# Kernel optimization log

Measured on AMD Instinct MI355X. Metric: run time of the kernel, lower is better.

## Reference

```python
import jax, jax.numpy as jnp
import numpy as np

N = 20000      # total nodes (20 proteins x 1000 residues)
E = 320000     # edges (avg degree 16)
F_IN = 22      # amino-acid feature dim
H = 4          # attention heads
C = 64         # hidden dim per head
HC = H * C     # 256
G = 20         # number of graphs
OUT = 128      # output embedding dim
NEG_SLOPE = 0.2


def setup_inputs() -> dict:
    key = jax.random.key(0)
    ks = jax.random.split(key, 24)
    x = jax.random.normal(ks[0], (N, F_IN), dtype=jnp.float32)
    edge_index = jax.random.randint(ks[1], (2, E), 0, N)
    batch = jnp.arange(N, dtype=jnp.int64) // (N // G)  # 1000 nodes per graph
    s = 0.1
    d = {
        'x': x, 'edge_index': edge_index, 'batch': batch,
        'Win': jax.random.normal(ks[2], (F_IN, C)) * s,
        'bin_': jnp.zeros((C,), jnp.float32),
        'Wout': jax.random.normal(ks[3], (2 * HC, OUT)) * s,
        'bout': jnp.zeros((OUT,), jnp.float32),
    }
    kidx = 4
    for i in range(3):
        in_dim = C if i == 0 else HC
        d[f'Wl{i}'] = jax.random.normal(ks[kidx], (in_dim, HC)) * s; kidx += 1
        d[f'Wr{i}'] = jax.random.normal(ks[kidx], (in_dim, HC)) * s; kidx += 1
        d[f'att{i}'] = jax.random.normal(ks[kidx], (H, C)) * s; kidx += 1
        d[f'b{i}'] = jnp.zeros((HC,), jnp.float32)
    return d


def _gatv2_layer(h, src, dst, Wl, Wr, att, bias):
    # PyG GATv2Conv (share_weights=False, concat=True), dropout off (eval)
    xl = (h @ Wl).reshape(-1, H, C)   # source transform (x_j)
    xr = (h @ Wr).reshape(-1, H, C)   # target transform (x_i)
    e = jax.nn.leaky_relu(xl[src] + xr[dst], NEG_SLOPE)  # [E+N, H, C]
    logit = jnp.einsum('ehc,hc->eh', e, att)             # [E+N, H]
    mx = jax.ops.segment_max(logit, dst, num_segments=N)
    mx = jnp.where(jnp.isfinite(mx), mx, 0.0)
    ex = jnp.exp(logit - mx[dst])
    den = jax.ops.segment_sum(ex, dst, num_segments=N)
    alpha = ex / (den[dst] + 1e-16)                      # segment softmax
    out = jax.ops.segment_sum(alpha[:, :, None] * xl[src], dst, num_segments=N)
    return out.reshape(-1, HC) + bias


def reference(x, edge_index, batch, Win, bin_,
              Wl0, Wr0, att0, b0, Wl1, Wr1, att1, b1, Wl2, Wr2, att2, b2,
              Wout, bout):
    # add self-loops once (add_self_loops=True in every GATv2Conv)
    loops = jnp.arange(N, dtype=edge_index.dtype)
    src = jnp.concatenate([edge_index[0], loops])
    dst = jnp.concatenate([edge_index[1], loops])

    h = jax.nn.relu(x @ Win + bin_)  # input_proj + ReLU (dropout = eval identity)
    layers = [(Wl0, Wr0, att0, b0), (Wl1, Wr1, att1, b1), (Wl2, Wr2, att2, b2)]
    for (Wl, Wr, att, b) in layers:
        h_prev = h
        h = jax.nn.elu(_gatv2_layer(h, src, dst, Wl, Wr, att, b))
        if h_prev.shape[-1] == h.shape[-1]:  # residual when dims match (layers 1,2)
            h = h + h_prev

    counts = jax.ops.segment_sum(jnp.ones((N,), h.dtype), batch, num_segments=G)
    x_mean = jax.ops.segment_sum(h, batch, num_segments=G) / counts[:, None]
    x_max = jax.ops.segment_max(h, batch, num_segments=G)
    x_global = jnp.concatenate([x_mean, x_max], axis=-1)  # [G, 512]
    return x_global @ Wout + bout                          # [G, 128]
```

## Files before the change

### kernel.cpp

```cpp
#include <hip/hip_runtime.h>
#include <hip/hip_bf16.h>
#include <math.h>

#define N_NODES 20000
#define N_EDGES 320000
#define F_IN 22
#define H_HEADS 4
#define C_DIM 64
#define HC 256
#define G_GRAPHS 20
#define OUT_DIM 128
#define NODES_PER_G 1000
#define POOL_CHUNKS 8
#define NODES_PER_CHUNK (NODES_PER_G / POOL_CHUNKS)
#define SCAN_NB ((N_NODES + 255) / 256)

typedef unsigned short ushortT;
typedef __attribute__((ext_vector_type(8))) short short8;
typedef __attribute__((ext_vector_type(4))) float v4f;

__device__ inline ushortT f2bf(float f) {
    unsigned int u = __float_as_uint(f);
    unsigned int r = (u + 0x7fffu + ((u >> 16) & 1u)) >> 16;
    return (ushortT)r;
}

__device__ inline float4 unpack_bf4(uint2 u) {
    float4 f;
    f.x = __uint_as_float(u.x << 16);
    f.y = __uint_as_float(u.x & 0xffff0000u);
    f.z = __uint_as_float(u.y << 16);
    f.w = __uint_as_float(u.y & 0xffff0000u);
    return f;
}


__global__ void hist_kernel(const int* __restrict__ dst, int* __restrict__ cnt, int e) {
    int i = blockIdx.x * blockDim.x + threadIdx.x;
    if (i < e) atomicAdd(&cnt[dst[i]], 1);
}

__global__ __launch_bounds__(256) void scanA_kernel(const int* __restrict__ cnt,
                                                    int* __restrict__ bsum) {
    __shared__ int red[256];
    int b = blockIdx.x, t = threadIdx.x;
    int i = b * 256 + t;
    red[t] = (i < N_NODES) ? cnt[i] : 0;
    __syncthreads();
    for (int s = 128; s > 0; s >>= 1) {
        if (t < s) red[t] += red[t + s];
        __syncthreads();
    }
    if (t == 0) bsum[b] = red[0];
}

__global__ __launch_bounds__(128) void scanB_kernel(const int* __restrict__ bsum,
                                                    int* __restrict__ bbase) {
    __shared__ int sc[128];
    int t = threadIdx.x;
    int v = (t < SCAN_NB) ? bsum[t] : 0;
    sc[t] = v;
    __syncthreads();
    for (int d = 1; d < 128; d <<= 1) {
        int u = (t >= d) ? sc[t - d] : 0;
        __syncthreads();
        sc[t] += u;
        __syncthreads();
    }
    if (t < SCAN_NB) bbase[t] = sc[t] - v;
}

__global__ __launch_bounds__(256) void scanC_kernel(const int* __restrict__ cnt,
                                                    const int* __restrict__ bbase,
                                                    int* __restrict__ off) {
    __shared__ int sc[256];
    int b = blockIdx.x, t = threadIdx.x;
    int i = b * 256 + t;
    int v = (i < N_NODES) ? cnt[i] : 0;
    sc[t] = v;
    __syncthreads();
    for (int d = 1; d < 256; d <<= 1) {
        int u = (t >= d) ? sc[t - d] : 0;
        __syncthreads();
        sc[t] += u;
        __syncthreads();
    }
    if (i < N_NODES) off[i] = bbase[b] + sc[t] - v;
}

__global__ void scatter_kernel(const int* __restrict__ src, const int* __restrict__ dst,
                               const int* __restrict__ off, int* __restrict__ fill,
                               int* __restrict__ csr, int e) {
    int i = blockIdx.x * blockDim.x + threadIdx.x;
    if (i < e) {
        int d = dst[i];
        int p = atomicAdd(&fill[d], 1);
        csr[off[d] + p] = src[i];
    }
}

__global__ __launch_bounds__(256) void wconv_kernel(
        const float* __restrict__ Wl0, const float* __restrict__ Wr0,
        const float* __restrict__ Wl1, const float* __restrict__ Wr1,
        const float* __restrict__ Wl2, const float* __restrict__ Wr2,
        ushortT* __restrict__ Bt0, ushortT* __restrict__ Bt1, ushortT* __restrict__ Bt2) {
    int z = blockIdx.z;
    int layer = z >> 1, isR = z & 1;
    const float* src; ushortT* dst; int K;
    if (layer == 0)      { K = 64;  dst = Bt0; src = isR ? Wr0 : Wl0; }
    else if (layer == 1) { K = 256; dst = Bt1; src = isR ? Wr1 : Wl1; }
    else                 { K = 256; dst = Bt2; src = isR ? Wr2 : Wl2; }
    int kx = blockIdx.y * 32;
    if (kx >= K) return;
    int nx = blockIdx.x * 32;
    __shared__ float tile[32][33];
    int t = threadIdx.x;
    int c = t & 31, r8 = t >> 5;
#pragma unroll
    for (int i = 0; i < 4; i++) {
        int kk = r8 + i * 8;
        tile[kk][c] = src[(kx + kk) * 256 + nx + c];
    }
    __syncthreads();
    int nbase = isR ? 256 : 0;
#pragma unroll
    for (int i = 0; i < 4; i++) {
        int nn = r8 + i * 8;
        dst[(size_t)(nbase + nx + nn) * K + kx + c] = f2bf(tile[c][nn]);
    }
}

__global__ void inproj_kernel(const float* __restrict__ x, const float* __restrict__ Win,
                              const float* __restrict__ bin, ushortT* __restrict__ h0b) {
    int tid = threadIdx.x;
    int node = blockIdx.x * 4 + (tid >> 6);
    int c = tid & 63;
    float acc = bin[c];
    const float* xr = x + node * F_IN;
#pragma unroll
    for (int f = 0; f < F_IN; f++) acc += xr[f] * Win[f * C_DIM + c];
    h0b[node * C_DIM + c] = f2bf(acc > 0.f ? acc : 0.f);
}

#define GBM 128
#define GBN 128
#define GBK 32
#define LDK 40

__global__ __launch_bounds__(256) void gemm_mfma_kernel(
        const ushortT* __restrict__ A, const ushortT* __restrict__ Bt,
        ushortT* __restrict__ XLb, ushortT* __restrict__ XRb, int M, int K) {
    __shared__ ushortT As[GBM * LDK];
    __shared__ ushortT Bs[GBN * LDK];
    int tid = threadIdx.x;
    int wave = tid >> 6, lane = tid & 63;
    int wm = wave & 1, wn = wave >> 1;
    int bm0 = blockIdx.y * GBM;
    int bn0 = blockIdx.x * GBN;

    v4f acc[4][4];
#pragma unroll
    for (int mt = 0; mt < 4; mt++)
#pragma unroll
        for (int nt = 0; nt < 4; nt++) acc[mt][nt] = (v4f){0.f, 0.f, 0.f, 0.f};

    int lrow = tid >> 2;
    int lkk = (tid & 3) * 8;

    for (int k0 = 0; k0 < K; k0 += GBK) {
#pragma unroll
        for (int h = 0; h < 2; h++) {
            int r = lrow + h * 64;
            int rg = bm0 + r; if (rg >= M) rg = 0;
            *(int4*)&As[r * LDK + lkk] = *(const int4*)&A[(size_t)rg * K + k0 + lkk];
            *(int4*)&Bs[r * LDK + lkk] = *(const int4*)&Bt[(size_t)(bn0 + r) * K + k0 + lkk];
        }
        __syncthreads();
        short8 af[4], bf[4];
        int mrow = lane & 15;
        int koff = (lane >> 4) * 8;
#pragma unroll
        for (int mt = 0; mt < 4; mt++)
            af[mt] = *(const short8*)&As[(wm * 64 + mt * 16 + mrow) * LDK + koff];
#pragma unroll
        for (int nt = 0; nt < 4; nt++)
            bf[nt] = *(const short8*)&Bs[(wn * 64 + nt * 16 + mrow) * LDK + koff];
#pragma unroll
        for (int mt = 0; mt < 4; mt++)
#pragma unroll
            for (int nt = 0; nt < 4; nt++)
                acc[mt][nt] = __builtin_amdgcn_mfma_f32_16x16x32_bf16(af[mt], bf[nt], acc[mt][nt], 0, 0, 0);
        __syncthreads();
    }

    int cbase = bn0 + wn * 64;
    ushortT* dst = XLb;
    if (cbase >= 256) { dst = XRb; cbase -= 256; }
    int col = cbase + (lane & 15);
    int rbase = bm0 + wm * 64 + ((lane >> 4) * 4);
#pragma unroll
    for (int mt = 0; mt < 4; mt++) {
#pragma unroll
        for (int reg = 0; reg < 4; reg++) {
            int row = rbase + mt * 16 + reg;
            if (row < M) {
#pragma unroll
                for (int nt = 0; nt < 4; nt++)
                    dst[(size_t)row * 256 + col + nt * 16] = f2bf(acc[mt][nt][reg]);
            }
        }
    }
}

__device__ inline void gat_edge(uint2 curu, const float4& xrv, const float4& attv,
                                float& den, float4& acc) {
    float4 xlv = unpack_bf4(curu);
    float t0 = xlv.x + xrv.x, t1 = xlv.y + xrv.y;
    float t2 = xlv.z + xrv.z, t3 = xlv.w + xrv.w;
    t0 = t0 > 0.f ? t0 : 0.2f * t0;
    t1 = t1 > 0.f ? t1 : 0.2f * t1;
    t2 = t2 > 0.f ? t2 : 0.2f * t2;
    t3 = t3 > 0.f ? t3 : 0.2f * t3;
    float p = t0 * attv.x + t1 * attv.y + t2 * attv.z + t3 * attv.w;
    p += __shfl_xor(p, 1, 64);
    p += __shfl_xor(p, 2, 64);
    p += __shfl_xor(p, 4, 64);
    p += __shfl_xor(p, 8, 64);
    p = fminf(p, 110.f);
    float w = exp2f(p);
    den += w;
    acc.x = fmaf(w, xlv.x, acc.x);
    acc.y = fmaf(w, xlv.y, acc.y);
    acc.z = fmaf(w, xlv.z, acc.z);
    acc.w = fmaf(w, xlv.w, acc.w);
}

__global__ __launch_bounds__(256) void gat_layer_kernel(
        const ushortT* __restrict__ xlb, const ushortT* __restrict__ xrb,
        const int* __restrict__ csr, const int* __restrict__ off,
        const int* __restrict__ cnt, const float* __restrict__ att,
        const float* __restrict__ bias, const float* __restrict__ hprev,
        float* __restrict__ hout, ushortT* __restrict__ houtb) {
    int lane = threadIdx.x & 63;
    int d = blockIdx.x * 4 + (threadIdx.x >> 6);

    const uint2* xl2 = (const uint2*)xlb;
    float4 xrv = unpack_bf4(((const uint2*)xrb)[d * 64 + lane]);
    float4 attv = ((const float4*)att)[lane];
    const float LOG2E = 1.44269504088896f;
    attv.x *= LOG2E; attv.y *= LOG2E; attv.z *= LOG2E; attv.w *= LOG2E;

    int start = off[d], deg = cnt[d];
    int M = deg + 1;

    int sa = (0 < deg) ? csr[start] : d;
    uint2 ra = xl2[sa * 64 + lane];
    int sb = (1 < deg) ? csr[start + 1] : d;
    uint2 rb = (M > 1) ? xl2[sb * 64 + lane] : ra;
    int na = (2 < deg) ? csr[start + 2] : d;
    int nb = (3 < deg) ? csr[start + 3] : d;

    float den = 0.f;
    float4 acc = {0.f, 0.f, 0.f, 0.f};

    int j = 0;
    for (; j + 2 <= M; j += 2) {
        uint2 ca = ra;
        ra = xl2[na * 64 + lane];
        int nna = (j + 4 < deg) ? csr[start + j + 4] : d;
        gat_edge(ca, xrv, attv, den, acc);

        uint2 cb = rb;
        rb = xl2[nb * 64 + lane];
        int nnb = (j + 5 < deg) ? csr[start + j + 5] : d;
        gat_edge(cb, xrv, attv, den, acc);

        na = nna; nb = nnb;
    }
    if (j < M) gat_edge(ra, xrv, attv, den, acc);

    float inv = 1.f / (den + 1e-16f);
    float4 bv = ((const float4*)bias)[lane];
    float4 v;
    v.x = acc.x * inv + bv.x;
    v.y = acc.y * inv + bv.y;
    v.z = acc.z * inv + bv.z;
    v.w = acc.w * inv + bv.w;
    v.x = v.x > 0.f ? v.x : __expf(v.x) - 1.f;
    v.y = v.y > 0.f ? v.y : __expf(v.y) - 1.f;
    v.z = v.z > 0.f ? v.z : __expf(v.z) - 1.f;
    v.w = v.w > 0.f ? v.w : __expf(v.w) - 1.f;
    if (hprev) {
        float4 hp = ((const float4*)hprev)[d * 64 + lane];
        v.x += hp.x; v.y += hp.y; v.z += hp.z; v.w += hp.w;
    }
    ((float4*)hout)[d * 64 + lane] = v;
    uint2 pb;
    pb.x = (unsigned int)f2bf(v.x) | ((unsigned int)f2bf(v.y) << 16);
    pb.y = (unsigned int)f2bf(v.z) | ((unsigned int)f2bf(v.w) << 16);
    ((uint2*)houtb)[d * 64 + lane] = pb;
}

__global__ __launch_bounds__(256) void pool_partial_kernel(
        const float* __restrict__ h, float* __restrict__ psum, float* __restrict__ pmax) {
    int blk = blockIdx.x;
    int tid = threadIdx.x;
    int g = blk / POOL_CHUNKS;
    int ch = blk % POOL_CHUNKS;
    const float* base = h + ((size_t)g * NODES_PER_G + ch * NODES_PER_CHUNK) * HC;
    float sum = 0.f, mx = -INFINITY;
    for (int n = 0; n < NODES_PER_CHUNK; n++) {
        float v = base[n * HC + tid];
        sum += v;
        mx = fmaxf(mx, v);
    }
    psum[blk * HC + tid] = sum;
    pmax[blk * HC + tid] = mx;
}

__global__ __launch_bounds__(256) void pool_out_kernel(
        const float* __restrict__ psum, const float* __restrict__ pmax,
        const float* __restrict__ Wout, const float* __restrict__ bout,
        float* __restrict__ out) {
    int g = blockIdx.x;
    int tid = threadIdx.x;
    __shared__ float xg[2 * HC];
    float sum = 0.f, mx = -INFINITY;
    for (int c = 0; c < POOL_CHUNKS; c++) {
        sum += psum[(g * POOL_CHUNKS + c) * HC + tid];
        mx = fmaxf(mx, pmax[(g * POOL_CHUNKS + c) * HC + tid]);
    }
    xg[tid] = sum * (1.0f / NODES_PER_G);
    xg[HC + tid] = mx;
    __syncthreads();
    if (tid < OUT_DIM) {
        float acc = bout[tid];
        for (int j = 0; j < 2 * HC; j++) acc += xg[j] * Wout[j * OUT_DIM + tid];
        out[g * OUT_DIM + tid] = acc;
    }
}


extern "C" void kernel_launch(void* const* d_in, const int* in_sizes, int n_in,
                              void* d_out, int out_size, void* d_ws, size_t ws_size,
                              hipStream_t stream) {
    const float* x    = (const float*)d_in[0];
    const int*   ei   = (const int*)d_in[1];
    const float* Win  = (const float*)d_in[3];
    const float* bin  = (const float*)d_in[4];
    const float* Wout = (const float*)d_in[5];
    const float* bout = (const float*)d_in[6];
    const float* Wl[3] = {(const float*)d_in[7],  (const float*)d_in[11], (const float*)d_in[15]};
    const float* Wr[3] = {(const float*)d_in[8],  (const float*)d_in[12], (const float*)d_in[16]};
    const float* att[3] = {(const float*)d_in[9], (const float*)d_in[13], (const float*)d_in[17]};
    const float* bb[3] = {(const float*)d_in[10], (const float*)d_in[14], (const float*)d_in[18]};
    float* out = (float*)d_out;

    const int* esrc = ei;
    const int* edst = ei + N_EDGES;

    float* hA   = (float*)d_ws;
    float* hB   = hA + (size_t)N_NODES * HC;
    float* psum = hB + (size_t)N_NODES * HC;
    float* pmax = psum + (size_t)G_GRAPHS * POOL_CHUNKS * HC;
    ushortT* h0b = (ushortT*)(pmax + (size_t)G_GRAPHS * POOL_CHUNKS * HC);
    ushortT* hAb = h0b + (size_t)N_NODES * C_DIM;
    ushortT* hBb = hAb + (size_t)N_NODES * HC;
    ushortT* XLb = hBb + (size_t)N_NODES * HC;
    ushortT* XRb = XLb + (size_t)N_NODES * HC;
    ushortT* Bt0 = XRb + (size_t)N_NODES * HC;
    ushortT* Bt1 = Bt0 + 512 * 64;
    ushortT* Bt2 = Bt1 + 512 * 256;
    int* cnt   = (int*)(Bt2 + 512 * 256);
    int* off   = cnt + N_NODES;
    int* fill  = off + N_NODES;
    int* csr   = fill + N_NODES;
    int* bsum  = csr + N_EDGES;
    int* bbase = bsum + SCAN_NB;

    hipMemsetAsync(cnt, 0, N_NODES * sizeof(int), stream);
    hipMemsetAsync(fill, 0, N_NODES * sizeof(int), stream);

    int eb = (N_EDGES + 255) / 256;
    hist_kernel<<<eb, 256, 0, stream>>>(edst, cnt, N_EDGES);
    scanA_kernel<<<SCAN_NB, 256, 0, stream>>>(cnt, bsum);
    scanB_kernel<<<1, 128, 0, stream>>>(bsum, bbase);
    scanC_kernel<<<SCAN_NB, 256, 0, stream>>>(cnt, bbase, off);
    scatter_kernel<<<eb, 256, 0, stream>>>(esrc, edst, off, fill, csr, N_EDGES);

    wconv_kernel<<<dim3(8, 8, 6), 256, 0, stream>>>(Wl[0], Wr[0], Wl[1], Wr[1], Wl[2], Wr[2],
                                                    Bt0, Bt1, Bt2);
    inproj_kernel<<<N_NODES / 4, 256, 0, stream>>>(x, Win, bin, h0b);

    dim3 ggrid(512 / GBN, (N_NODES + GBM - 1) / GBM);

    gemm_mfma_kernel<<<ggrid, 256, 0, stream>>>(h0b, Bt0, XLb, XRb, N_NODES, C_DIM);
    gat_layer_kernel<<<N_NODES / 4, 256, 0, stream>>>(XLb, XRb, csr, off, cnt, att[0], bb[0],
                                                      nullptr, hA, hAb);

    gemm_mfma_kernel<<<ggrid, 256, 0, stream>>>(hAb, Bt1, XLb, XRb, N_NODES, HC);
    gat_layer_kernel<<<N_NODES / 4, 256, 0, stream>>>(XLb, XRb, csr, off, cnt, att[1], bb[1],
                                                      hA, hB, hBb);

    gemm_mfma_kernel<<<ggrid, 256, 0, stream>>>(hBb, Bt2, XLb, XRb, N_NODES, HC);
    gat_layer_kernel<<<N_NODES / 4, 256, 0, stream>>>(XLb, XRb, csr, off, cnt, att[2], bb[2],
                                                      hB, hA, hAb);

    pool_partial_kernel<<<G_GRAPHS * POOL_CHUNKS, 256, 0, stream>>>(hA, psum, pmax);
    pool_out_kernel<<<G_GRAPHS, 256, 0, stream>>>(psum, pmax, Wout, bout, out);
}
```

Before: 312.4 us.

## Split GAT wave into two edge halves with 16-byte loads; prefetch GEMM tiles

Result: slower. 350.6 us (+12.2%).

```diff
diff --git a/kernel.cpp b/kernel.cpp
--- a/kernel.cpp
+++ b/kernel.cpp
@@ -25,12 +25,12 @@
     return (ushortT)r;
 }
 
-__device__ inline float4 unpack_bf4(uint2 u) {
+__device__ inline float4 unpack_bf4(unsigned int lo, unsigned int hi) {
     float4 f;
-    f.x = __uint_as_float(u.x << 16);
-    f.y = __uint_as_float(u.x & 0xffff0000u);
-    f.z = __uint_as_float(u.y << 16);
-    f.w = __uint_as_float(u.y & 0xffff0000u);
+    f.x = __uint_as_float(lo << 16);
+    f.y = __uint_as_float(lo & 0xffff0000u);
+    f.z = __uint_as_float(hi << 16);
+    f.w = __uint_as_float(hi & 0xffff0000u);
     return f;
 }
 
@@ -167,15 +167,38 @@
     int lrow = tid >> 2;
     int lkk = (tid & 3) * 8;
 
+    int rg0[2];
+#pragma unroll
+    for (int h = 0; h < 2; h++) {
+        int rg = bm0 + lrow + h * 64; if (rg >= M) rg = 0;
+        rg0[h] = rg;
+    }
+
+    int4 pa[2], pb[2];
+#pragma unroll
+    for (int h = 0; h < 2; h++) {
+        int r = lrow + h * 64;
+        pa[h] = *(const int4*)&A[(size_t)rg0[h] * K + lkk];
+        pb[h] = *(const int4*)&Bt[(size_t)(bn0 + r) * K + lkk];
+    }
+
     for (int k0 = 0; k0 < K; k0 += GBK) {
 #pragma unroll
         for (int h = 0; h < 2; h++) {
             int r = lrow + h * 64;
-            int rg = bm0 + r; if (rg >= M) rg = 0;
-            *(int4*)&As[r * LDK + lkk] = *(const int4*)&A[(size_t)rg * K + k0 + lkk];
-            *(int4*)&Bs[r * LDK + lkk] = *(const int4*)&Bt[(size_t)(bn0 + r) * K + k0 + lkk];
+            *(int4*)&As[r * LDK + lkk] = pa[h];
+            *(int4*)&Bs[r * LDK + lkk] = pb[h];
         }
         __syncthreads();
+        if (k0 + GBK < K) {
+            int k1 = k0 + GBK;
+#pragma unroll
+            for (int h = 0; h < 2; h++) {
+                int r = lrow + h * 64;
+                pa[h] = *(const int4*)&A[(size_t)rg0[h] * K + k1 + lkk];
+                pb[h] = *(const int4*)&Bt[(size_t)(bn0 + r) * K + k1 + lkk];
+            }
+        }
         short8 af[4], bf[4];
         int mrow = lane & 15;
         int koff = (lane >> 4) * 8;
@@ -210,29 +233,6 @@
             }
         }
     }
-}
-
-__device__ inline void gat_edge(uint2 curu, const float4& xrv, const float4& attv,
-                                float& den, float4& acc) {
-    float4 xlv = unpack_bf4(curu);
-    float t0 = xlv.x + xrv.x, t1 = xlv.y + xrv.y;
-    float t2 = xlv.z + xrv.z, t3 = xlv.w + xrv.w;
-    t0 = t0 > 0.f ? t0 : 0.2f * t0;
-    t1 = t1 > 0.f ? t1 : 0.2f * t1;
-    t2 = t2 > 0.f ? t2 : 0.2f * t2;
-    t3 = t3 > 0.f ? t3 : 0.2f * t3;
-    float p = t0 * attv.x + t1 * attv.y + t2 * attv.z + t3 * attv.w;
-    p += __shfl_xor(p, 1, 64);
-    p += __shfl_xor(p, 2, 64);
-    p += __shfl_xor(p, 4, 64);
-    p += __shfl_xor(p, 8, 64);
-    p = fminf(p, 110.f);
-    float w = exp2f(p);
-    den += w;
-    acc.x = fmaf(w, xlv.x, acc.x);
-    acc.y = fmaf(w, xlv.y, acc.y);
-    acc.z = fmaf(w, xlv.z, acc.z);
-    acc.w = fmaf(w, xlv.w, acc.w);
 }
 
 __global__ __launch_bounds__(256) void gat_layer_kernel(
@@ -241,64 +241,119 @@
         const int* __restrict__ cnt, const float* __restrict__ att,
         const float* __restrict__ bias, const float* __restrict__ hprev,
         float* __restrict__ hout, ushortT* __restrict__ houtb) {
-    int lane = threadIdx.x & 63;
-    int d = blockIdx.x * 4 + (threadIdx.x >> 6);
-
-    const uint2* xl2 = (const uint2*)xlb;
-    float4 xrv = unpack_bf4(((const uint2*)xrb)[d * 64 + lane]);
-    float4 attv = ((const float4*)att)[lane];
+    int tid = threadIdx.x;
+    int lane = tid & 63;
+    int d = blockIdx.x * 4 + (tid >> 6);
+    int half = lane >> 5;
+    int sl = lane & 31;
+
+    const uint4* xl4 = (const uint4*)xlb;
+    uint4 xru = ((const uint4*)xrb)[d * 32 + sl];
+    float4 xr0 = unpack_bf4(xru.x, xru.y);
+    float4 xr1 = unpack_bf4(xru.z, xru.w);
     const float LOG2E = 1.44269504088896f;
-    attv.x *= LOG2E; attv.y *= LOG2E; attv.z *= LOG2E; attv.w *= LOG2E;
+    float4 at0 = ((const float4*)att)[sl * 2];
+    float4 at1 = ((const float4*)att)[sl * 2 + 1];
+    at0.x *= LOG2E; at0.y *= LOG2E; at0.z *= LOG2E; at0.w *= LOG2E;
+    at1.x *= LOG2E; at1.y *= LOG2E; at1.z *= LOG2E; at1.w *= LOG2E;
 
     int start = off[d], deg = cnt[d];
     int M = deg + 1;
-
-    int sa = (0 < deg) ? csr[start] : d;
-    uint2 ra = xl2[sa * 64 + lane];
-    int sb = (1 < deg) ? csr[start + 1] : d;
-    uint2 rb = (M > 1) ? xl2[sb * 64 + lane] : ra;
-    int na = (2 < deg) ? csr[start + 2] : d;
-    int nb = (3 < deg) ? csr[start + 3] : d;
+    int P = (M + 1) >> 1;
+
+    int s0 = (half < deg) ? csr[start + half] : d;
+    uint4 r0 = xl4[s0 * 32 + sl];
+    int e1 = half + 2;
+    int s1 = (e1 < deg) ? csr[start + e1] : d;
+    uint4 r1 = xl4[s1 * 32 + sl];
+    int e2 = half + 4;
+    int sn = (e2 < deg) ? csr[start + e2] : d;
 
     float den = 0.f;
-    float4 acc = {0.f, 0.f, 0.f, 0.f};
-
-    int j = 0;
-    for (; j + 2 <= M; j += 2) {
-        uint2 ca = ra;
-        ra = xl2[na * 64 + lane];
-        int nna = (j + 4 < deg) ? csr[start + j + 4] : d;
-        gat_edge(ca, xrv, attv, den, acc);
-
-        uint2 cb = rb;
-        rb = xl2[nb * 64 + lane];
-        int nnb = (j + 5 < deg) ? csr[start + j + 5] : d;
-        gat_edge(cb, xrv, attv, den, acc);
-
-        na = nna; nb = nnb;
-    }
-    if (j < M) gat_edge(ra, xrv, attv, den, acc);
+    float4 a0 = {0.f, 0.f, 0.f, 0.f}, a1 = {0.f, 0.f, 0.f, 0.f};
+
+    for (int j = 0; j < P; j++) {
+        int e = 2 * j + half;
+        uint4 cur = r0;
+        r0 = r1;
+        r1 = xl4[sn * 32 + sl];
+        int en = 2 * j + half + 6;
+        sn = (en < deg) ? csr[start + en] : d;
+
+        float4 x0 = unpack_bf4(cur.x, cur.y);
+        float4 x1 = unpack_bf4(cur.z, cur.w);
+        float t0 = x0.x + xr0.x, t1 = x0.y + xr0.y, t2 = x0.z + xr0.z, t3 = x0.w + xr0.w;
+        float t4 = x1.x + xr1.x, t5 = x1.y + xr1.y, t6 = x1.z + xr1.z, t7 = x1.w + xr1.w;
+        t0 = t0 > 0.f ? t0 : 0.2f * t0;
+        t1 = t1 > 0.f ? t1 : 0.2f * t1;
+        t2 = t2 > 0.f ? t2 : 0.2f * t2;
+        t3 = t3 > 0.f ? t3 : 0.2f * t3;
+        t4 = t4 > 0.f ? t4 : 0.2f * t4;
+        t5 = t5 > 0.f ? t5 : 0.2f * t5;
+        t6 = t6 > 0.f ? t6 : 0.2f * t6;
+        t7 = t7 > 0.f ? t7 : 0.2f * t7;
+        float p = t0 * at0.x + t1 * at0.y + t2 * at0.z + t3 * at0.w
+                + t4 * at1.x + t5 * at1.y + t6 * at1.z + t7 * at1.w;
+        p += __shfl_xor(p, 1, 64);
+        p += __shfl_xor(p, 2, 64);
+        p += __shfl_xor(p, 4, 64);
+        p = fminf(p, 110.f);
+        float w = exp2f(p);
+        if (e >= M) w = 0.f;
+        den += w;
+        a0.x = fmaf(w, x0.x, a0.x);
+        a0.y = fmaf(w, x0.y, a0.y);
+        a0.z = fmaf(w, x0.z, a0.z);
+        a0.w = fmaf(w, x0.w, a0.w);
+        a1.x = fmaf(w, x1.x, a1.x);
+        a1.y = fmaf(w, x1.y, a1.y);
+        a1.z = fmaf(w, x1.z, a1.z);
+        a1.w = fmaf(w, x1.w, a1.w);
+    }
+
+    den += __shfl_xor(den, 32, 64);
+    a0.x += __shfl_xor(a0.x, 32, 64);
+    a0.y += __shfl_xor(a0.y, 32, 64);
+    a0.z += __shfl_xor(a0.z, 32, 64);
+    a0.w += __shfl_xor(a0.w, 32, 64);
+    a1.x += __shfl_xor(a1.x, 32, 64);
+    a1.y += __shfl_xor(a1.y, 32, 64);
+    a1.z += __shfl_xor(a1.z, 32, 64);
+    a1.w += __shfl_xor(a1.w, 32, 64);
 
     float inv = 1.f / (den + 1e-16f);
-    float4 bv = ((const float4*)bias)[lane];
-    float4 v;
-    v.x = acc.x * inv + bv.x;
-    v.y = acc.y * inv + bv.y;
-    v.z = acc.z * inv + bv.z;
-    v.w = acc.w * inv + bv.w;
-    v.x = v.x > 0.f ? v.x : __expf(v.x) - 1.f;
-    v.y = v.y > 0.f ? v.y : __expf(v.y) - 1.f;
-    v.z = v.z > 0.f ? v.z : __expf(v.z) - 1.f;
-    v.w = v.w > 0.f ? v.w : __expf(v.w) - 1.f;
+    float4 b0 = ((const float4*)bias)[sl * 2];
+    float4 b1 = ((const float4*)bias)[sl * 2 + 1];
+    float4 v0, v1;
+    v0.x = a0.x * inv + b0.x;  v0.y = a0.y * inv + b0.y;
+    v0.z = a0.z * inv + b0.z;  v0.w = a0.w * inv + b0.w;
+    v1.x = a1.x * inv + b1.x;  v1.y = a1.y * inv + b1.y;
+    v1.z = a1.z * inv + b1.z;  v1.w = a1.w * inv + b1.w;
+    v0.x = v0.x > 0.f ? v0.x : __expf(v0.x) - 1.f;
+    v0.y = v0.y > 0.f ? v0.y : __expf(v0.y) - 1.f;
+    v0.z = v0.z > 0.f ? v0.z : __expf(v0.z) - 1.f;
+    v0.w = v0.w > 0.f ? v0.w : __expf(v0.w) - 1.f;
+    v1.x = v1.x > 0.f ? v1.x : __expf(v1.x) - 1.f;
+    v1.y = v1.y > 0.f ? v1.y : __expf(v1.y) - 1.f;
+    v1.z = v1.z > 0.f ? v1.z : __expf(v1.z) - 1.f;
+    v1.w = v1.w > 0.f ? v1.w : __expf(v1.w) - 1.f;
     if (hprev) {
-        float4 hp = ((const float4*)hprev)[d * 64 + lane];
-        v.x += hp.x; v.y += hp.y; v.z += hp.z; v.w += hp.w;
-    }
-    ((float4*)hout)[d * 64 + lane] = v;
-    uint2 pb;
-    pb.x = (unsigned int)f2bf(v.x) | ((unsigned int)f2bf(v.y) << 16);
-    pb.y = (unsigned int)f2bf(v.z) | ((unsigned int)f2bf(v.w) << 16);
-    ((uint2*)houtb)[d * 64 + lane] = pb;
+        float4 hp0 = ((const float4*)hprev)[d * 64 + sl * 2];
+        float4 hp1 = ((const float4*)hprev)[d * 64 + sl * 2 + 1];
+        v0.x += hp0.x; v0.y += hp0.y; v0.z += hp0.z; v0.w += hp0.w;
+        v1.x += hp1.x; v1.y += hp1.y; v1.z += hp1.z; v1.w += hp1.w;
+    }
+    if (half == 0) {
+        ((float4*)hout)[d * 64 + sl * 2] = v0;
+        ((float4*)hout)[d * 64 + sl * 2 + 1] = v1;
+    } else {
+        uint4 pbv;
+        pbv.x = (unsigned int)f2bf(v0.x) | ((unsigned int)f2bf(v0.y) << 16);
+        pbv.y = (unsigned int)f2bf(v0.z) | ((unsigned int)f2bf(v0.w) << 16);
+        pbv.z = (unsigned int)f2bf(v1.x) | ((unsigned int)f2bf(v1.y) << 16);
+        pbv.w = (unsigned int)f2bf(v1.z) | ((unsigned int)f2bf(v1.w) << 16);
+        ((uint4*)houtb)[d * 32 + sl] = pbv;
+    }
 }
 
 __global__ __launch_bounds__(256) void pool_partial_kernel(
```
